# Performance work log

Measured on AMD Instinct MI355X. Metric: run time of the kernel, lower is better.

The kernel has to match this reference:

```python
import jax, jax.numpy as jnp
import numpy as np

K = 5
PAD = (K - 1) // 2
EPS_NORM = 1e-8
MASS_BOUND = 1e-7


def _window_indices(H, W):
    # For each output location (y,x) and each offset (dy,dx) in the kxk window,
    # compute the flat index of (y+dy, x+dx) in prev space and a validity mask.
    ys, xs = jnp.meshgrid(jnp.arange(H), jnp.arange(W), indexing='ij')  # [H,W]
    offs = jnp.arange(-PAD, PAD + 1)
    dy, dx = jnp.meshgrid(offs, offs, indexing='ij')  # [k,k]
    py = ys[:, :, None, None] + dy[None, None]  # [H,W,k,k]
    px = xs[:, :, None, None] + dx[None, None]
    valid = (py >= 0) & (py < H) & (px >= 0) & (px < W)
    ploc = jnp.clip(py, 0, H - 1) * W + jnp.clip(px, 0, W - 1)
    HW, KK = H * W, K * K
    return ploc.reshape(HW, KK), valid.reshape(HW, KK)


def setup_inputs() -> dict:
    key = jax.random.key(0)
    k1, k2, k3 = jax.random.split(key, 3)
    N, D, H, W = 8, 64, 64, 64
    return {
        'cur_feat': jax.random.normal(k1, (N, D, H, W), dtype=jnp.float32),
        'prev_feat': jax.random.normal(k2, (N, D, H, W), dtype=jnp.float32),
        'prev_mem': jax.random.normal(k3, (N, D, H, W), dtype=jnp.float32),
    }


def reference(cur_feat, prev_feat, prev_mem):
    N, D, H, W = prev_mem.shape
    HW = H * W
    cur = cur_feat.reshape(N, -1, HW)   # [N,Dc,HW]
    prev = prev_feat.reshape(N, -1, HW)
    # torch.norm(x, 0) = number of nonzero entries (scalar per batch)
    nc = jnp.sum(cur != 0, axis=(1, 2)).astype(cur.dtype) + EPS_NORM   # [N]
    npv = jnp.sum(prev != 0, axis=(1, 2)).astype(prev.dtype) + EPS_NORM
    # full cost volume: [N, HW(cur loc), HW(prev loc)], negatives clamped to 0
    aff = jnp.einsum('ndp,ndq->npq', cur, prev) / (nc * npv)[:, None, None]
    aff = jnp.maximum(aff, 0.0)

    ploc, valid = _window_indices(H, W)        # [HW,KK]
    loc = jnp.arange(HW)[:, None]              # [HW,1]
    coef = aff[:, loc, ploc] * valid[None].astype(aff.dtype)  # [N,HW,KK]
    mass = jnp.sum(coef, axis=-1)              # [N,HW]
    zero_mass = jnp.abs(mass) < MASS_BOUND
    w = coef / jnp.where(zero_mass, 1.0, mass)[:, :, None]    # [N,HW,KK]

    pm = prev_mem.reshape(N, D, HW)            # [N,D,HW]
    pm_win = pm[:, :, ploc]                    # [N,D,HW,KK]
    val = jnp.einsum('npk,ndpk->ndp', w, pm_win)  # weighted aggregation
    out = jnp.where(zero_mass[:, None, :], pm, val)  # mass==0 -> passthrough
    return out.reshape(N, D, H, W)
```

## Files before the change

### kernel.cpp

```cpp
#include <hip/hip_runtime.h>

#define N_  8
#define D_  64
#define H_  64
#define W_  64
#define HW_ (H_ * W_)
#define KK  25

__global__ __launch_bounds__(256) void count_nz_kernel(
    const float4* __restrict__ cur, const float4* __restrict__ prev,
    const float4* __restrict__ pmv,
    unsigned int* __restrict__ pc, unsigned int* __restrict__ pq,
    unsigned int* __restrict__ pr)
{
    __shared__ unsigned int sc[4], sp[4], sr[4];
    const int t    = threadIdx.x;
    const int wid  = t >> 6;
    const int lane = t & 63;

    unsigned int wc = 0, wp = 0, wr = 0;
#pragma unroll
    for (int j = 0; j < 4; ++j) {
        int idx = blockIdx.x * 1024 + j * 256 + t;
        float4 a = cur[idx];
        float4 b = prev[idx];
        float4 m = pmv[idx];
        wc += (unsigned)__popcll(__ballot(a.x != 0.f));
        wc += (unsigned)__popcll(__ballot(a.y != 0.f));
        wc += (unsigned)__popcll(__ballot(a.z != 0.f));
        wc += (unsigned)__popcll(__ballot(a.w != 0.f));
        wp += (unsigned)__popcll(__ballot(b.x != 0.f));
        wp += (unsigned)__popcll(__ballot(b.y != 0.f));
        wp += (unsigned)__popcll(__ballot(b.z != 0.f));
        wp += (unsigned)__popcll(__ballot(b.w != 0.f));
        wr += (unsigned)__popcll(__ballot(m.x != 0.f));
        wr += (unsigned)__popcll(__ballot(m.y != 0.f));
        wr += (unsigned)__popcll(__ballot(m.z != 0.f));
        wr += (unsigned)__popcll(__ballot(m.w != 0.f));
    }
    if (lane == 0) { sc[wid] = wc; sp[wid] = wp; sr[wid] = wr; }
    __syncthreads();
    if (t == 0) {
        pc[blockIdx.x] = sc[0] + sc[1] + sc[2] + sc[3];
        pq[blockIdx.x] = sp[0] + sp[1] + sp[2] + sp[3];
        pr[blockIdx.x] = sr[0] + sr[1] + sr[2] + sr[3];
    }
}

__global__ __launch_bounds__(512, 1) void feature_align_kernel(
    const float* __restrict__ cur, const float* __restrict__ prev,
    const float* __restrict__ pm, float* __restrict__ out,
    const unsigned int* __restrict__ pc, const unsigned int* __restrict__ pq)
{
    __shared__ float red[4][KK][128];

    const int b    = blockIdx.x;
    const int n    = b >> 5;
    const int y0   = (b & 31) * 2;
    const int lane = threadIdx.x & 63;
    const int dg   = __builtin_amdgcn_readfirstlane(threadIdx.x >> 6);
    const int r    = lane >> 5;
    const int xq   = lane & 31;
    const int x0   = xq * 2;
    const int y    = y0 + r;
    const int pix0 = r * 64 + x0;

    int cb[3];
#pragma unroll
    for (int i = 0; i < 3; ++i)
        cb[i] = min(max(x0 - 2 + 2 * i, 0), W_ - 2);
    unsigned voff[5][3];
#pragma unroll
    for (int ky = 0; ky < 5; ++ky) {
        int qy = min(max(y + ky - 2, 0), H_ - 1);
#pragma unroll
        for (int i = 0; i < 3; ++i)
            voff[ky][i] = (unsigned)((qy * W_ + cb[i]) * 4);
    }
    const unsigned curoff = (unsigned)((y * W_ + x0) * 4);

    const size_t nbase = (size_t)n * D_ * HW_;
    const char* curb  = (const char*)(cur  + nbase + (size_t)dg * 8 * HW_);
    const char* prevb = (const char*)(prev + nbase + (size_t)dg * 8 * HW_);
    const char* pmb   = (const char*)(pm   + nbase + (size_t)dg * 8 * HW_);
    char*       outb  = (char*)(out + nbase + (size_t)dg * 8 * HW_);

    float2 pmc[8];
#pragma unroll
    for (int dd = 0; dd < 8; ++dd)
        pmc[dd] = *(const float2*)(pmb + (size_t)dd * HW_ * 4 + curoff);
    unsigned int ccnt = pc[(n << 6) + lane];
    unsigned int vcnt = pq[(n << 6) + lane];

    float acc0[KK], acc1[KK];
#pragma unroll
    for (int k = 0; k < KK; ++k) { acc0[k] = 0.f; acc1[k] = 0.f; }

#pragma unroll
    for (int dd = 0; dd < 8; ++dd) {
        const char* cch = curb  + (size_t)dd * HW_ * 4;
        const char* pch = prevb + (size_t)dd * HW_ * 4;
        float2 c = *(const float2*)(cch + curoff);
        float2 t[5][3];
#pragma unroll
        for (int ky = 0; ky < 5; ++ky)
#pragma unroll
            for (int i = 0; i < 3; ++i)
                t[ky][i] = *(const float2*)(pch + voff[ky][i]);
#pragma unroll
        for (int ky = 0; ky < 5; ++ky) {
            float v[6] = { t[ky][0].x, t[ky][0].y, t[ky][1].x,
                           t[ky][1].y, t[ky][2].x, t[ky][2].y };
#pragma unroll
            for (int kx = 0; kx < 5; ++kx) {
                acc0[ky * 5 + kx] = fmaf(c.x, v[kx],     acc0[ky * 5 + kx]);
                acc1[ky * 5 + kx] = fmaf(c.y, v[kx + 1], acc1[ky * 5 + kx]);
            }
        }
    }

    if (dg < 4) {
#pragma unroll
        for (int k = 0; k < KK; ++k)
            *(float2*)&red[dg][k][pix0] = make_float2(acc0[k], acc1[k]);
    }
    __syncthreads();
    if (dg >= 4) {
#pragma unroll
        for (int k = 0; k < KK; ++k) {
            float2 t2 = *(float2*)&red[dg - 4][k][pix0];
            t2.x += acc0[k]; t2.y += acc1[k];
            *(float2*)&red[dg - 4][k][pix0] = t2;
        }
    }
    __syncthreads();

    if (threadIdx.x < 128) {
        const int pix = threadIdx.x;
        const int rr  = pix >> 6;
        const int xx  = pix & 63;

        unsigned int cc = ccnt, vv = vcnt;
#pragma unroll
        for (int s = 32; s >= 1; s >>= 1) {
            cc += __shfl_xor(cc, s);
            vv += __shfl_xor(vv, s);
        }
        float scale = 1.0f / (((float)cc + 1e-8f) * ((float)vv + 1e-8f));

        float mass = 0.f;
        float cf[KK];
#pragma unroll
        for (int k = 0; k < KK; ++k) {
            float s = red[0][k][pix] + red[1][k][pix]
                    + red[2][k][pix] + red[3][k][pix];
            int ky = k / 5, kx = k % 5;
            int py  = y0 + rr + ky - 2;
            int pxc = xx + kx - 2;
            bool val = (py >= 0) && (py < H_) && (pxc >= 0) && (pxc < W_);
            float c = val ? fmaxf(s * scale, 0.f) : 0.f;
            cf[k] = c;
            mass += c;
        }
        bool  zero = fabsf(mass) < 1e-7f;
        float inv  = zero ? 0.f : 1.0f / mass;
#pragma unroll
        for (int k = 0; k < KK; ++k) red[0][k][pix] = cf[k] * inv;
        red[1][0][pix] = zero ? 1.f : 0.f;
    }
    __syncthreads();

    const float zf0 = red[1][0][pix0];
    const float zf1 = red[1][0][pix0 + 1];

    if (zf0 != 0.f && zf1 != 0.f) {
#pragma unroll
        for (int dd = 0; dd < 8; ++dd)
            *(float2*)(outb + (size_t)dd * HW_ * 4 + curoff) = pmc[dd];
    } else {
        float w0[KK], w1[KK];
#pragma unroll
        for (int k = 0; k < KK; ++k) {
            float2 ww = *(float2*)&red[0][k][pix0];
            w0[k] = ww.x; w1[k] = ww.y;
        }
#pragma unroll
        for (int dd = 0; dd < 8; ++dd) {
            const char* pch = pmb + (size_t)dd * HW_ * 4;
            float2 t2[5][3];
#pragma unroll
            for (int ky = 0; ky < 5; ++ky)
#pragma unroll
                for (int i = 0; i < 3; ++i)
                    t2[ky][i] = *(const float2*)(pch + voff[ky][i]);
            float v0 = 0.f, v1 = 0.f;
#pragma unroll
            for (int ky = 0; ky < 5; ++ky) {
                float v[6] = { t2[ky][0].x, t2[ky][0].y, t2[ky][1].x,
                               t2[ky][1].y, t2[ky][2].x, t2[ky][2].y };
#pragma unroll
                for (int kx = 0; kx < 5; ++kx) {
                    v0 = fmaf(w0[ky * 5 + kx], v[kx],     v0);
                    v1 = fmaf(w1[ky * 5 + kx], v[kx + 1], v1);
                }
            }
            float2 o;
            o.x = (zf0 != 0.f) ? pmc[dd].x : v0;
            o.y = (zf1 != 0.f) ? pmc[dd].y : v1;
            *(float2*)(outb + (size_t)dd * HW_ * 4 + curoff) = o;
        }
    }
}

extern "C" void kernel_launch(void* const* d_in, const int* in_sizes, int n_in,
                              void* d_out, int out_size, void* d_ws, size_t ws_size,
                              hipStream_t stream)
{
    const float* cur  = (const float*)d_in[0];
    const float* prev = (const float*)d_in[1];
    const float* pm   = (const float*)d_in[2];
    float*       out  = (float*)d_out;
    unsigned int* pc  = (unsigned int*)d_ws;
    unsigned int* pq  = pc + 512;
    unsigned int* pr  = pq + 512;

    count_nz_kernel<<<512, 256, 0, stream>>>(
        (const float4*)cur, (const float4*)prev, (const float4*)pm, pc, pq, pr);

    feature_align_kernel<<<256, 512, 0, stream>>>(cur, prev, pm, out, pc, pq);
}
```

Baseline: 86.48 us.

## Fuse nonzero counting into align kernel via cross-block tagged slot handshake

Drops the separate count-nonzero pass. Each block now counts nonzeros of cur and prev over its own rows while it loads them, publishes the counts to global slots with tagged release stores, and spin-waits on the 32 slots of its batch before normalizing. The scale multiply is folded into the zero-mass threshold, and blocks are remapped so that one batch's row blocks are spread across IDs. This avoids a second full pass over all three inputs and one kernel launch. In exchange it depends on all 256 blocks being co-resident (launch bounds now allow 2 per CU) and on stale workspace tags not matching, which risks deadlock or reading stale values.

```diff
diff --git a/kernel.cpp b/kernel.cpp
--- a/kernel.cpp
+++ b/kernel.cpp
@@ -7,56 +7,22 @@
 #define HW_ (H_ * W_)
 #define KK  25
 
-__global__ __launch_bounds__(256) void count_nz_kernel(
-    const float4* __restrict__ cur, const float4* __restrict__ prev,
-    const float4* __restrict__ pmv,
-    unsigned int* __restrict__ pc, unsigned int* __restrict__ pq,
-    unsigned int* __restrict__ pr)
-{
-    __shared__ unsigned int sc[4], sp[4], sr[4];
-    const int t    = threadIdx.x;
-    const int wid  = t >> 6;
-    const int lane = t & 63;
-
-    unsigned int wc = 0, wp = 0, wr = 0;
-#pragma unroll
-    for (int j = 0; j < 4; ++j) {
-        int idx = blockIdx.x * 1024 + j * 256 + t;
-        float4 a = cur[idx];
-        float4 b = prev[idx];
-        float4 m = pmv[idx];
-        wc += (unsigned)__popcll(__ballot(a.x != 0.f));
-        wc += (unsigned)__popcll(__ballot(a.y != 0.f));
-        wc += (unsigned)__popcll(__ballot(a.z != 0.f));
-        wc += (unsigned)__popcll(__ballot(a.w != 0.f));
-        wp += (unsigned)__popcll(__ballot(b.x != 0.f));
-        wp += (unsigned)__popcll(__ballot(b.y != 0.f));
-        wp += (unsigned)__popcll(__ballot(b.z != 0.f));
-        wp += (unsigned)__popcll(__ballot(b.w != 0.f));
-        wr += (unsigned)__popcll(__ballot(m.x != 0.f));
-        wr += (unsigned)__popcll(__ballot(m.y != 0.f));
-        wr += (unsigned)__popcll(__ballot(m.z != 0.f));
-        wr += (unsigned)__popcll(__ballot(m.w != 0.f));
-    }
-    if (lane == 0) { sc[wid] = wc; sp[wid] = wp; sr[wid] = wr; }
-    __syncthreads();
-    if (t == 0) {
-        pc[blockIdx.x] = sc[0] + sc[1] + sc[2] + sc[3];
-        pq[blockIdx.x] = sp[0] + sp[1] + sp[2] + sp[3];
-        pr[blockIdx.x] = sr[0] + sr[1] + sr[2] + sr[3];
-    }
-}
-
-__global__ __launch_bounds__(512, 1) void feature_align_kernel(
+#define TAGC 0x69000000u
+#define TAGP 0x96000000u
+
+__global__ __launch_bounds__(512, 2) void feature_align_fused(
     const float* __restrict__ cur, const float* __restrict__ prev,
     const float* __restrict__ pm, float* __restrict__ out,
-    const unsigned int* __restrict__ pc, const unsigned int* __restrict__ pq)
+    unsigned int* __restrict__ slots)
 {
     __shared__ float red[4][KK][128];
-
-    const int b    = blockIdx.x;
-    const int n    = b >> 5;
-    const int y0   = (b & 31) * 2;
+    __shared__ unsigned int scnt[8][2];
+
+    const int bid  = blockIdx.x;
+    const int bb   = ((bid & 7) << 5) | (bid >> 3);
+    const int n    = bb >> 5;
+    const int yp   = bb & 31;
+    const int y0   = yp * 2;
     const int lane = threadIdx.x & 63;
     const int dg   = __builtin_amdgcn_readfirstlane(threadIdx.x >> 6);
     const int r    = lane >> 5;
@@ -89,13 +55,12 @@
 #pragma unroll
     for (int dd = 0; dd < 8; ++dd)
         pmc[dd] = *(const float2*)(pmb + (size_t)dd * HW_ * 4 + curoff);
-    unsigned int ccnt = pc[(n << 6) + lane];
-    unsigned int vcnt = pq[(n << 6) + lane];
 
     float acc0[KK], acc1[KK];
 #pragma unroll
     for (int k = 0; k < KK; ++k) { acc0[k] = 0.f; acc1[k] = 0.f; }
 
+    unsigned int cntc = 0, cntp = 0;
 #pragma unroll
     for (int dd = 0; dd < 8; ++dd) {
         const char* cch = curb  + (size_t)dd * HW_ * 4;
@@ -107,6 +72,12 @@
 #pragma unroll
             for (int i = 0; i < 3; ++i)
                 t[ky][i] = *(const float2*)(pch + voff[ky][i]);
+
+        cntc += (unsigned)__popcll(__ballot(c.x != 0.f));
+        cntc += (unsigned)__popcll(__ballot(c.y != 0.f));
+        cntp += (unsigned)__popcll(__ballot(t[2][1].x != 0.f));
+        cntp += (unsigned)__popcll(__ballot(t[2][1].y != 0.f));
+
 #pragma unroll
         for (int ky = 0; ky < 5; ++ky) {
             float v[6] = { t[ky][0].x, t[ky][0].y, t[ky][1].x,
@@ -118,6 +89,7 @@
             }
         }
     }
+    if (lane == 0) { scnt[dg][0] = cntc; scnt[dg][1] = cntp; }
 
     if (dg < 4) {
 #pragma unroll
@@ -125,6 +97,16 @@
             *(float2*)&red[dg][k][pix0] = make_float2(acc0[k], acc1[k]);
     }
     __syncthreads();
+
+    if (threadIdx.x == 0) {
+        unsigned int tc = 0, tp = 0;
+#pragma unroll
+        for (int j = 0; j < 8; ++j) { tc += scnt[j][0]; tp += scnt[j][1]; }
+        __hip_atomic_store(&slots[n * 32 + yp],       TAGC | tc,
+                           __ATOMIC_RELEASE, __HIP_MEMORY_SCOPE_AGENT);
+        __hip_atomic_store(&slots[256 + n * 32 + yp], TAGP | tp,
+                           __ATOMIC_RELEASE, __HIP_MEMORY_SCOPE_AGENT);
+    }
     if (dg >= 4) {
 #pragma unroll
         for (int k = 0; k < KK; ++k) {
@@ -140,13 +122,24 @@
         const int rr  = pix >> 6;
         const int xx  = pix & 63;
 
-        unsigned int cc = ccnt, vv = vcnt;
-#pragma unroll
-        for (int s = 32; s >= 1; s >>= 1) {
+        const int sidx = n * 32 + (lane & 31);
+        unsigned int vC, vP;
+        do {
+            vC = __hip_atomic_load(&slots[sidx], __ATOMIC_ACQUIRE,
+                                   __HIP_MEMORY_SCOPE_AGENT);
+        } while ((vC & 0xFF000000u) != TAGC || (vC & 0x00FFFFFFu) > 8192u);
+        do {
+            vP = __hip_atomic_load(&slots[256 + sidx], __ATOMIC_ACQUIRE,
+                                   __HIP_MEMORY_SCOPE_AGENT);
+        } while ((vP & 0xFF000000u) != TAGP || (vP & 0x00FFFFFFu) > 8192u);
+        unsigned int cc = vC & 0x00FFFFFFu;
+        unsigned int vv = vP & 0x00FFFFFFu;
+#pragma unroll
+        for (int s = 16; s >= 1; s >>= 1) {
             cc += __shfl_xor(cc, s);
             vv += __shfl_xor(vv, s);
         }
-        float scale = 1.0f / (((float)cc + 1e-8f) * ((float)vv + 1e-8f));
+        const float thr = 1e-7f * ((float)cc + 1e-8f) * ((float)vv + 1e-8f);
 
         float mass = 0.f;
         float cf[KK];
@@ -158,11 +151,11 @@
             int py  = y0 + rr + ky - 2;
             int pxc = xx + kx - 2;
             bool val = (py >= 0) && (py < H_) && (pxc >= 0) && (pxc < W_);
-            float c = val ? fmaxf(s * scale, 0.f) : 0.f;
+            float c = val ? fmaxf(s, 0.f) : 0.f;
             cf[k] = c;
             mass += c;
         }
-        bool  zero = fabsf(mass) < 1e-7f;
+        bool  zero = mass < thr;
         float inv  = zero ? 0.f : 1.0f / mass;
 #pragma unroll
         for (int k = 0; k < KK; ++k) red[0][k][pix] = cf[k] * inv;
@@ -220,12 +213,7 @@
     const float* prev = (const float*)d_in[1];
     const float* pm   = (const float*)d_in[2];
     float*       out  = (float*)d_out;
-    unsigned int* pc  = (unsigned int*)d_ws;
-    unsigned int* pq  = pc + 512;
-    unsigned int* pr  = pq + 512;
-
-    count_nz_kernel<<<512, 256, 0, stream>>>(
-        (const float4*)cur, (const float4*)prev, (const float4*)pm, pc, pq, pr);
-
-    feature_align_kernel<<<256, 512, 0, stream>>>(cur, prev, pm, out, pc, pq);
+    unsigned int* slots = (unsigned int*)d_ws;
+
+    feature_align_fused<<<256, 512, 0, stream>>>(cur, prev, pm, out, slots);
 }
```

Result: slower. 122.4 us (+41.5%).
